# Optimization experiments

Measured on AMD Instinct MI355X. Metric: run time of the kernel, lower is better.

Reference implementation:

```python
import jax, jax.numpy as jnp
import numpy as np

C_CURV = 1.0  # hyperbolic curvature (init kwarg c)
EPS = 1e-7


def _to_ball(v, max_norm=0.8):
    # rescale rows to lie strictly inside the unit Poincare ball
    n = jnp.linalg.norm(v, axis=-1, keepdims=True)
    return v * (max_norm / (n + 1.0))


def setup_inputs() -> dict:
    key = jax.random.key(0)
    k1, k2 = jax.random.split(key)
    B, C, D = 32768, 2048, 512
    z_mix = _to_ball(jax.random.normal(k1, (B, D), dtype=jnp.float32))
    prototypes = _to_ball(jax.random.normal(k2, (C, D), dtype=jnp.float32))
    repel_margin = jnp.float32(2.0)
    return {"z_mix": z_mix, "prototypes": prototypes, "repel_margin": repel_margin}


def dist_matrix(x, y, c):
    # Poincare-ball pairwise distance (arccosh form):
    # d(x,y) = arccosh(1 + 2c||x-y||^2 / ((1-c||x||^2)(1-c||y||^2))) / sqrt(c)
    x2 = jnp.sum(x * x, axis=-1)            # (B,)
    y2 = jnp.sum(y * y, axis=-1)            # (C,)
    xy = jnp.einsum('bd,cd->bc', x, y)      # (B, C)
    sqdist = jnp.maximum(x2[:, None] + y2[None, :] - 2.0 * xy, 0.0)
    denom = (1.0 - c * x2)[:, None] * (1.0 - c * y2)[None, :]
    arg = 1.0 + 2.0 * c * sqdist / jnp.maximum(denom, EPS)
    return jnp.arccosh(jnp.maximum(arg, 1.0 + EPS)) / jnp.sqrt(c)


def reference(z_mix, prototypes, repel_margin):
    dist2proto = dist_matrix(z_mix, prototypes, C_CURV)   # (B, C)
    min_dist = jnp.min(dist2proto, axis=1)                # (B,)
    return jnp.mean(jax.nn.relu(repel_margin - min_dist))
```

## Files before the change

kernel.cpp:

```cpp
#include <hip/hip_runtime.h>
#include <stdint.h>

#define EPS_F 1e-7f

typedef float f32x4 __attribute__((ext_vector_type(4)));
typedef int   v8i   __attribute__((ext_vector_type(8)));

union A32 { uint4 u4[2]; v8i v; };

__device__ __forceinline__ unsigned cvt4(float a, float b, float c, float d) {
  int v = __builtin_amdgcn_cvt_pk_fp8_f32(a, b, 0, false);
  return (unsigned)__builtin_amdgcn_cvt_pk_fp8_f32(c, d, v, true);
}

#define MFMA128(A, B, C) __builtin_amdgcn_mfma_scale_f32_16x16x128_f8f6f4( \
    (A), (B), (C), 0, 0, 0, 0x7F7F7F7F, 0, 0x7F7F7F7F)


__global__ __launch_bounds__(256) void prep_kernel(
    const float* __restrict__ protos, uint8_t* __restrict__ wsB,
    float* __restrict__ y2a, float* __restrict__ rya,
    float* __restrict__ out) {
  const int lane = threadIdx.x & 63;
  const int w    = threadIdx.x >> 6;
  const int c    = blockIdx.x * 4 + w;
  const int g    = c >> 4, cl = c & 15;
  const float4* p = (const float4*)(protos + (size_t)c * 512 + lane * 8);
  float4 f0 = p[0], f1 = p[1];
  float s = f0.x*f0.x + f0.y*f0.y + f0.z*f0.z + f0.w*f0.w
          + f1.x*f1.x + f1.y*f1.y + f1.z*f1.z + f1.w*f1.w;
#pragma unroll
  for (int off = 32; off > 0; off >>= 1) s += __shfl_xor(s, off, 64);
  if (lane == 0) { y2a[c] = s; rya[c] = 1.f / (1.f - s); }
  unsigned ux = cvt4(f0.x, f0.y, f0.z, f0.w);
  unsigned uy = cvt4(f1.x, f1.y, f1.z, f1.w);
  const int kb = lane >> 4, kg = (lane >> 2) & 3, bo = lane & 3;
  size_t ri  = (size_t)(g * 4 + kb) * 64 + kg * 16 + cl;
  size_t off = ri * 16 + (size_t)(bo & 1) * 8 + (size_t)(bo >> 1) * (512u * 1024u);
  *(uint2*)(wsB + off) = make_uint2(ux, uy);
  if (blockIdx.x == 0 && threadIdx.x == 0) out[0] = 0.f;
}

__global__ __launch_bounds__(256, 1) void gemm_min_kernel(
    const float* __restrict__ z, const uint8_t* __restrict__ wsB,
    const float* __restrict__ y2a, const float* __restrict__ rya,
    const float* __restrict__ marg, float* __restrict__ out) {
  __shared__ uint4 As2[4096];
  __shared__ float x2s[128];
  __shared__ float rxs[128];
  __shared__ float minbuf[128][4];

  const int tid  = threadIdx.x;
  const int lane = tid & 63;
  const int w    = tid >> 6;
  const int q    = lane >> 4;
  const int l15  = lane & 15;
  const size_t rowbase = (size_t)blockIdx.x * 128;

  const uint4* BLo = (const uint4*)wsB;
  const uint4* BHi = BLo + 32768;

  A32 Bp0[2], Bp1[2];
#pragma unroll
  for (int i = 0; i < 2; ++i) {
    size_t r0 = (size_t)(w * 128 + i) * 64 + lane;
    Bp0[i].u4[0] = BLo[r0];       Bp0[i].u4[1] = BHi[r0];
    Bp1[i].u4[0] = BLo[r0 + 256]; Bp1[i].u4[1] = BHi[r0 + 256];
  }

  {
    const int c4 = lane & 3;
    const int m  = lane >> 2;
    const float* zb = z + (rowbase + w * 32) * 512 + lane * 4;
#pragma unroll
    for (int ss = 0; ss < 16; ++ss) {
      float4 f0 = *(const float4*)(zb + (2 * ss + 0) * 512);
      float4 f1 = *(const float4*)(zb + (2 * ss + 0) * 512 + 256);
      float4 f2 = *(const float4*)(zb + (2 * ss + 1) * 512);
      float4 f3 = *(const float4*)(zb + (2 * ss + 1) * 512 + 256);
      float sa = f0.x*f0.x + f0.y*f0.y + f0.z*f0.z + f0.w*f0.w
               + f1.x*f1.x + f1.y*f1.y + f1.z*f1.z + f1.w*f1.w;
      float sb = f2.x*f2.x + f2.y*f2.y + f2.z*f2.z + f2.w*f2.w
               + f3.x*f3.x + f3.y*f3.y + f3.z*f3.z + f3.w*f3.w;
#pragma unroll
      for (int off = 32; off > 0; off >>= 1) {
        sa += __shfl_xor(sa, off, 64);
        sb += __shfl_xor(sb, off, 64);
      }
      if (lane == 0) {
        int r0 = w * 32 + 2 * ss;
        x2s[r0] = sa;     rxs[r0] = 1.f / (1.f - sa);
        x2s[r0 + 1] = sb; rxs[r0 + 1] = 1.f / (1.f - sb);
      }
      unsigned v0 = cvt4(f0.x, f0.y, f0.z, f0.w);
      unsigned v1 = cvt4(f1.x, f1.y, f1.z, f1.w);
      unsigned v2 = cvt4(f2.x, f2.y, f2.z, f2.w);
      unsigned v3 = cvt4(f3.x, f3.y, f3.z, f3.w);
      unsigned t;
      t = (unsigned)__shfl_xor((int)((c4 & 1) ? v0 : v1), 1, 64);
      if (c4 & 1) v0 = t; else v1 = t;
      t = (unsigned)__shfl_xor((int)((c4 & 1) ? v2 : v3), 1, 64);
      if (c4 & 1) v2 = t; else v3 = t;
      t = (unsigned)__shfl_xor((int)((c4 & 2) ? v0 : v2), 2, 64);
      if (c4 & 2) v0 = t; else v2 = t;
      t = (unsigned)__shfl_xor((int)((c4 & 2) ? v1 : v3), 2, 64);
      if (c4 & 2) v1 = t; else v3 = t;
      int K   = ((c4 & 1) << 8) + (m << 4);
      int kb  = K >> 7;
      int kg  = (K >> 5) & 3;
      int pl  = (K >> 4) & 1;
      int rr  = 2 * ss + (c4 >> 1);
      int rf  = 2 * w + (rr >> 4);
      int r15 = rr & 15;
      int ri  = pl * 2048 + (kb * 8 + rf) * 64 + kg * 16 + r15;
      As2[ri] = make_uint4(v0, v1, v2, v3);
    }
  }
  __syncthreads();

  float x2r[8][4];
#pragma unroll
  for (int rf = 0; rf < 8; ++rf) {
    float4 x4 = *(const float4*)&x2s[rf * 16 + q * 4];
    x2r[rf][0] = x4.x; x2r[rf][1] = x4.y; x2r[rf][2] = x4.z; x2r[rf][3] = x4.w;
  }

  float tmin[8][4];
#pragma unroll
  for (int rf = 0; rf < 8; ++rf)
#pragma unroll
    for (int r = 0; r < 4; ++r) tmin[rf][r] = 3.4e38f;

  const float* y2p = y2a + w * 512 + l15;
  const float* ryp = rya + w * 512 + l15;

#pragma clang loop unroll(disable)
  for (int s = 0; s < 16; ++s) {
    f32x4 acc[8][2];
#pragma unroll
    for (int rf = 0; rf < 8; ++rf) {
      f32x4 z4 = {0.f, 0.f, 0.f, 0.f};
      acc[rf][0] = z4; acc[rf][1] = z4;
    }
    float y2v0 = y2p[s * 32],      ryv0 = ryp[s * 32];
    float y2v1 = y2p[s * 32 + 16], ryv1 = ryp[s * 32 + 16];

#pragma unroll
    for (int kb = 0; kb < 4; ++kb) {
      v8i bv0 = Bp0[kb & 1].v;
      v8i bv1 = Bp1[kb & 1].v;
      {
        int ip = s * 4 + kb + 2;
        size_t r0 = (size_t)(w * 128 + (ip >> 2) * 8 + (ip & 3)) * 64 + lane;
        Bp0[kb & 1].u4[0] = BLo[r0];       Bp0[kb & 1].u4[1] = BHi[r0];
        Bp1[kb & 1].u4[0] = BLo[r0 + 256]; Bp1[kb & 1].u4[1] = BHi[r0 + 256];
      }
#pragma unroll
      for (int rf = 0; rf < 8; ++rf) {
        A32 a;
        int ri = (kb * 8 + rf) * 64 + lane;
        a.u4[0] = As2[ri];
        a.u4[1] = As2[2048 + ri];
        acc[rf][0] = MFMA128(a.v, bv0, acc[rf][0]);
        acc[rf][1] = MFMA128(a.v, bv1, acc[rf][1]);
      }
    }

#pragma unroll
    for (int rf = 0; rf < 8; ++rf) {
#pragma unroll
      for (int r = 0; r < 4; ++r) {
        float xv = x2r[rf][r];
        float u0 = fmaxf(fmaf(-2.f, acc[rf][0][r], xv + y2v0), 0.f) * ryv0;
        float u1 = fmaxf(fmaf(-2.f, acc[rf][1][r], xv + y2v1), 0.f) * ryv1;
        tmin[rf][r] = fminf(tmin[rf][r], fminf(u0, u1));
      }
    }
  }

#pragma unroll
  for (int rf = 0; rf < 8; ++rf) {
#pragma unroll
    for (int r = 0; r < 4; ++r) {
      float v = tmin[rf][r];
      v = fminf(v, __shfl_xor(v, 1, 64));
      v = fminf(v, __shfl_xor(v, 2, 64));
      v = fminf(v, __shfl_xor(v, 4, 64));
      v = fminf(v, __shfl_xor(v, 8, 64));
      if (l15 == 0) minbuf[rf * 16 + q * 4 + r][w] = v;
    }
  }
  __syncthreads();

  if (w < 2) {
    int row = w * 64 + lane;
    float m = fminf(fminf(minbuf[row][0], minbuf[row][1]),
                    fminf(minbuf[row][2], minbuf[row][3]));
    float t = m * rxs[row];
    float arg = fmaxf(fmaf(2.f, t, 1.f), 1.f + EPS_F);
    float contrib = fmaxf(marg[0] - acoshf(arg), 0.f);
#pragma unroll
    for (int off = 32; off > 0; off >>= 1) contrib += __shfl_xor(contrib, off, 64);
    if (lane == 0) atomicAdd(out, contrib * (1.0f / 32768.f));
  }
}

extern "C" void kernel_launch(void* const* d_in, const int* in_sizes, int n_in,
                              void* d_out, int out_size, void* d_ws, size_t ws_size,
                              hipStream_t stream) {
  const float* z      = (const float*)d_in[0];
  const float* protos = (const float*)d_in[1];
  const float* marg   = (const float*)d_in[2];
  float* out = (float*)d_out;
  uint8_t* wsB = (uint8_t*)d_ws;
  float* y2a = (float*)((char*)d_ws + (1 << 20) + 192 * 1024);
  float* rya = y2a + 2048;

  prep_kernel<<<512, 256, 0, stream>>>(protos, wsB, y2a, rya, out);
  gemm_min_kernel<<<256, 256, 0, stream>>>(z, wsB, y2a, rya, marg, out);
}
```

Measured before the change: 135.8 us.

## Switch FP8 GEMM from 16x16x128 to 32x32x64 scaled MFMA with new layouts

Replaces the 16x16x128 scaled FP8 MFMA with the 32x32x64 variant. The prototype workspace layout, the LDS A-tile layout (with a rotation swizzle to avoid bank conflicts) and the epilogue min-reduction are all reworked to match the 32x32 output fragment. The larger MFMA shape raises the compute-to-operand ratio, so each wave issues fewer LDS and global B loads per FLOP. In exchange the accumulator state grows to 16 floats per tile and the layout indexing becomes more complex, with a risk of subtle mapping errors.

```diff
diff --git a/kernel.cpp b/kernel.cpp
--- a/kernel.cpp
+++ b/kernel.cpp
@@ -3,8 +3,8 @@
 
 #define EPS_F 1e-7f
 
-typedef float f32x4 __attribute__((ext_vector_type(4)));
-typedef int   v8i   __attribute__((ext_vector_type(8)));
+typedef float f32x16 __attribute__((ext_vector_type(16)));
+typedef int   v8i    __attribute__((ext_vector_type(8)));
 
 union A32 { uint4 u4[2]; v8i v; };
 
@@ -13,7 +13,7 @@
   return (unsigned)__builtin_amdgcn_cvt_pk_fp8_f32(c, d, v, true);
 }
 
-#define MFMA128(A, B, C) __builtin_amdgcn_mfma_scale_f32_16x16x128_f8f6f4( \
+#define MFMA3264(A, B, C) __builtin_amdgcn_mfma_scale_f32_32x32x64_f8f6f4( \
     (A), (B), (C), 0, 0, 0, 0x7F7F7F7F, 0, 0x7F7F7F7F)
 
 
@@ -24,7 +24,7 @@
   const int lane = threadIdx.x & 63;
   const int w    = threadIdx.x >> 6;
   const int c    = blockIdx.x * 4 + w;
-  const int g    = c >> 4, cl = c & 15;
+  const int g    = c >> 5, c31 = c & 31;
   const float4* p = (const float4*)(protos + (size_t)c * 512 + lane * 8);
   float4 f0 = p[0], f1 = p[1];
   float s = f0.x*f0.x + f0.y*f0.y + f0.z*f0.z + f0.w*f0.w
@@ -34,10 +34,9 @@
   if (lane == 0) { y2a[c] = s; rya[c] = 1.f / (1.f - s); }
   unsigned ux = cvt4(f0.x, f0.y, f0.z, f0.w);
   unsigned uy = cvt4(f1.x, f1.y, f1.z, f1.w);
-  const int kb = lane >> 4, kg = (lane >> 2) & 3, bo = lane & 3;
-  size_t ri  = (size_t)(g * 4 + kb) * 64 + kg * 16 + cl;
-  size_t off = ri * 16 + (size_t)(bo & 1) * 8 + (size_t)(bo >> 1) * (512u * 1024u);
-  *(uint2*)(wsB + off) = make_uint2(ux, uy);
+  const int kb = lane >> 3, hi = (lane >> 2) & 1, pp = (lane >> 1) & 1;
+  size_t ri  = ((size_t)(g * 8 + kb)) * 128 + hi * 64 + pp * 32 + c31;
+  *(uint2*)(wsB + ri * 16 + (lane & 1) * 8) = make_uint2(ux, uy);
   if (blockIdx.x == 0 && threadIdx.x == 0) out[0] = 0.f;
 }
 
@@ -45,7 +44,7 @@
     const float* __restrict__ z, const uint8_t* __restrict__ wsB,
     const float* __restrict__ y2a, const float* __restrict__ rya,
     const float* __restrict__ marg, float* __restrict__ out) {
-  __shared__ uint4 As2[4096];
+  __shared__ uint4 As[4096];
   __shared__ float x2s[128];
   __shared__ float rxs[128];
   __shared__ float minbuf[128][4];
@@ -53,19 +52,18 @@
   const int tid  = threadIdx.x;
   const int lane = tid & 63;
   const int w    = tid >> 6;
-  const int q    = lane >> 4;
-  const int l15  = lane & 15;
+  const int c31  = lane & 31;
+  const int hi   = lane >> 5;
   const size_t rowbase = (size_t)blockIdx.x * 128;
 
-  const uint4* BLo = (const uint4*)wsB;
-  const uint4* BHi = BLo + 32768;
-
-  A32 Bp0[2], Bp1[2];
+  const uint4* Bg = (const uint4*)wsB;
+
+  A32 Bp[2];
 #pragma unroll
   for (int i = 0; i < 2; ++i) {
-    size_t r0 = (size_t)(w * 128 + i) * 64 + lane;
-    Bp0[i].u4[0] = BLo[r0];       Bp0[i].u4[1] = BHi[r0];
-    Bp1[i].u4[0] = BLo[r0 + 256]; Bp1[i].u4[1] = BHi[r0 + 256];
+    size_t r0 = ((size_t)(w * 16) * 8 + i) * 128 + hi * 64 + c31;
+    Bp[i].u4[0] = Bg[r0];
+    Bp[i].u4[1] = Bg[r0 + 32];
   }
 
   {
@@ -105,89 +103,82 @@
       if (c4 & 2) v0 = t; else v2 = t;
       t = (unsigned)__shfl_xor((int)((c4 & 2) ? v1 : v3), 2, 64);
       if (c4 & 2) v1 = t; else v3 = t;
-      int K   = ((c4 & 1) << 8) + (m << 4);
-      int kb  = K >> 7;
-      int kg  = (K >> 5) & 3;
-      int pl  = (K >> 4) & 1;
-      int rr  = 2 * ss + (c4 >> 1);
-      int rf  = 2 * w + (rr >> 4);
-      int r15 = rr & 15;
-      int ri  = pl * 2048 + (kb * 8 + rf) * 64 + kg * 16 + r15;
-      As2[ri] = make_uint4(v0, v1, v2, v3);
+      int k16 = ((c4 & 1) << 4) + m;
+      int r31 = 2 * ss + (c4 >> 1);
+      int ri  = k16 * 128 + w * 32 + ((r31 + k16) & 31);
+      As[ri] = make_uint4(v0, v1, v2, v3);
     }
   }
   __syncthreads();
 
-  float x2r[8][4];
-#pragma unroll
-  for (int rf = 0; rf < 8; ++rf) {
-    float4 x4 = *(const float4*)&x2s[rf * 16 + q * 4];
-    x2r[rf][0] = x4.x; x2r[rf][1] = x4.y; x2r[rf][2] = x4.z; x2r[rf][3] = x4.w;
-  }
-
-  float tmin[8][4];
-#pragma unroll
-  for (int rf = 0; rf < 8; ++rf)
-#pragma unroll
-    for (int r = 0; r < 4; ++r) tmin[rf][r] = 3.4e38f;
-
-  const float* y2p = y2a + w * 512 + l15;
-  const float* ryp = rya + w * 512 + l15;
+  float tmin[4][16];
+#pragma unroll
+  for (int rf = 0; rf < 4; ++rf)
+#pragma unroll
+    for (int r = 0; r < 16; ++r) tmin[rf][r] = 3.4e38f;
+
+  const float* y2p = y2a + w * 512 + c31;
+  const float* ryp = rya + w * 512 + c31;
 
 #pragma clang loop unroll(disable)
   for (int s = 0; s < 16; ++s) {
-    f32x4 acc[8][2];
-#pragma unroll
-    for (int rf = 0; rf < 8; ++rf) {
-      f32x4 z4 = {0.f, 0.f, 0.f, 0.f};
-      acc[rf][0] = z4; acc[rf][1] = z4;
-    }
-    float y2v0 = y2p[s * 32],      ryv0 = ryp[s * 32];
-    float y2v1 = y2p[s * 32 + 16], ryv1 = ryp[s * 32 + 16];
-
-#pragma unroll
-    for (int kb = 0; kb < 4; ++kb) {
-      v8i bv0 = Bp0[kb & 1].v;
-      v8i bv1 = Bp1[kb & 1].v;
+    f32x16 acc[4];
+#pragma unroll
+    for (int rf = 0; rf < 4; ++rf) {
+      f32x16 zz = {0.f};
+      acc[rf] = zz;
+    }
+    float y2v = y2p[s * 32], ryv = ryp[s * 32];
+
+#pragma unroll
+    for (int kb = 0; kb < 8; ++kb) {
+      v8i bv = Bp[kb & 1].v;
       {
-        int ip = s * 4 + kb + 2;
-        size_t r0 = (size_t)(w * 128 + (ip >> 2) * 8 + (ip & 3)) * 64 + lane;
-        Bp0[kb & 1].u4[0] = BLo[r0];       Bp0[kb & 1].u4[1] = BHi[r0];
-        Bp1[kb & 1].u4[0] = BLo[r0 + 256]; Bp1[kb & 1].u4[1] = BHi[r0 + 256];
-      }
-#pragma unroll
-      for (int rf = 0; rf < 8; ++rf) {
+        int ip = s * 8 + kb + 2;
+        size_t r0 = ((size_t)(w * 16 + (ip >> 3)) * 8 + (ip & 7)) * 128
+                  + hi * 64 + c31;
+        Bp[kb & 1].u4[0] = Bg[r0];
+        Bp[kb & 1].u4[1] = Bg[r0 + 32];
+      }
+      const int k0 = kb * 4 + hi * 2;
+#pragma unroll
+      for (int rf = 0; rf < 4; ++rf) {
         A32 a;
-        int ri = (kb * 8 + rf) * 64 + lane;
-        a.u4[0] = As2[ri];
-        a.u4[1] = As2[2048 + ri];
-        acc[rf][0] = MFMA128(a.v, bv0, acc[rf][0]);
-        acc[rf][1] = MFMA128(a.v, bv1, acc[rf][1]);
-      }
-    }
-
-#pragma unroll
-    for (int rf = 0; rf < 8; ++rf) {
-#pragma unroll
-      for (int r = 0; r < 4; ++r) {
-        float xv = x2r[rf][r];
-        float u0 = fmaxf(fmaf(-2.f, acc[rf][0][r], xv + y2v0), 0.f) * ryv0;
-        float u1 = fmaxf(fmaf(-2.f, acc[rf][1][r], xv + y2v1), 0.f) * ryv1;
-        tmin[rf][r] = fminf(tmin[rf][r], fminf(u0, u1));
-      }
-    }
-  }
-
-#pragma unroll
-  for (int rf = 0; rf < 8; ++rf) {
-#pragma unroll
-    for (int r = 0; r < 4; ++r) {
+        a.u4[0] = As[(k0    ) * 128 + rf * 32 + ((c31 + k0    ) & 31)];
+        a.u4[1] = As[(k0 + 1) * 128 + rf * 32 + ((c31 + k0 + 1) & 31)];
+        acc[rf] = MFMA3264(a.v, bv, acc[rf]);
+      }
+    }
+
+#pragma unroll
+    for (int rf = 0; rf < 4; ++rf) {
+#pragma unroll
+      for (int rg = 0; rg < 4; ++rg) {
+        float4 x4 = *(const float4*)&x2s[rf * 32 + rg * 8 + hi * 4];
+        float u0 = fmaxf(fmaf(-2.f, acc[rf][rg * 4 + 0], x4.x + y2v), 0.f) * ryv;
+        float u1 = fmaxf(fmaf(-2.f, acc[rf][rg * 4 + 1], x4.y + y2v), 0.f) * ryv;
+        float u2 = fmaxf(fmaf(-2.f, acc[rf][rg * 4 + 2], x4.z + y2v), 0.f) * ryv;
+        float u3 = fmaxf(fmaf(-2.f, acc[rf][rg * 4 + 3], x4.w + y2v), 0.f) * ryv;
+        tmin[rf][rg * 4 + 0] = fminf(tmin[rf][rg * 4 + 0], u0);
+        tmin[rf][rg * 4 + 1] = fminf(tmin[rf][rg * 4 + 1], u1);
+        tmin[rf][rg * 4 + 2] = fminf(tmin[rf][rg * 4 + 2], u2);
+        tmin[rf][rg * 4 + 3] = fminf(tmin[rf][rg * 4 + 3], u3);
+      }
+    }
+  }
+
+#pragma unroll
+  for (int rf = 0; rf < 4; ++rf) {
+#pragma unroll
+    for (int r = 0; r < 16; ++r) {
       float v = tmin[rf][r];
       v = fminf(v, __shfl_xor(v, 1, 64));
       v = fminf(v, __shfl_xor(v, 2, 64));
       v = fminf(v, __shfl_xor(v, 4, 64));
       v = fminf(v, __shfl_xor(v, 8, 64));
-      if (l15 == 0) minbuf[rf * 16 + q * 4 + r][w] = v;
+      v = fminf(v, __shfl_xor(v, 16, 64));
+      if (c31 == 0)
+        minbuf[rf * 32 + (r & 3) + 8 * (r >> 2) + 4 * hi][w] = v;
     }
   }
   __syncthreads();
```

Result: slower. 150.2 us (+10.6%).
